# Performance work log

Measured on AMD Instinct MI355X. Metric: run time of the kernel, lower is better.

## Reference

```python
import jax, jax.numpy as jnp
from jax import lax
import numpy as np

N, T, HID, COMB, ATT, K, D = 128, 64, 512, 1024, 128, 20, 2
FMAP = 64  # CNN output channels; feature map is 14x14 -> 196 locations
ODIM = K + 2 * K * D + K + 1  # 121 mixture-density output params


def setup_inputs() -> dict:
    key = jax.random.key(0)
    keys = iter(jax.random.split(key, 64))

    def rn(shape, s=0.05):
        return jax.random.normal(next(keys), shape, jnp.float32) * s

    inp = dict(
        x=rn((N, T, D), 1.0),
        x_canv=jax.random.uniform(next(keys), (N, 1, 28, 28), dtype=jnp.float32),
        start=rn((N, D), 1.0),
        conv1_w=rn((16, 1, 3, 3), 0.3), conv1_b=rn((16,)),
        conv2_w=rn((32, 16, 3, 3), 0.1), conv2_b=rn((32,)),
        conv3_w=rn((64, 32, 3, 3), 0.1), conv3_b=rn((64,)),
        init_w=rn((2 * HID, FMAP + 16)), init_b=rn((2 * HID,)),
        Uw=rn((ATT, HID)), Ub=rn((ATT,)),
        Ww=rn((ATT, FMAP)), Wb=rn((ATT,)),
        vw=rn((1, ATT)), vb=rn((1,)),
        beta_w=rn((FMAP, HID)), beta_b=rn((FMAP,)),
        xemb_w=rn((16, D), 0.5), xemb_b=rn((16,)),
        semb_w=rn((16, D), 0.5), semb_b=rn((16,)),
        Wih=rn((4 * HID, FMAP + 16)), Whh=rn((4 * HID, HID)),
        bih=rn((4 * HID,)), bhh=rn((4 * HID,)),
        comb_w=rn((COMB, FMAP + HID + 32)), comb_b=rn((COMB,)),
        out_w=rn((ODIM, COMB)), out_b=rn((ODIM,)),
    )
    return inp


def _conv(x, w, b, stride):
    # torch Conv2d(kernel=3, padding=1) with NCHW / OIHW layout
    y = lax.conv_general_dilated(x, w, (stride, stride), ((1, 1), (1, 1)),
                                 dimension_numbers=('NCHW', 'OIHW', 'NCHW'))
    return y + b[None, :, None, None]


def reference(x, x_canv, start, conv1_w, conv1_b, conv2_w, conv2_b, conv3_w, conv3_b,
              init_w, init_b, Uw, Ub, Ww, Wb, vw, vb, beta_w, beta_b,
              xemb_w, xemb_b, semb_w, semb_b, Wih, Whh, bih, bhh,
              comb_w, comb_b, out_w, out_b):
    n, Tt, d = x.shape
    # sequence_pad: prepend zero vector, drop last step
    xp = jnp.concatenate([jnp.zeros((n, 1, d), x.dtype), x[:, :-1]], axis=1)
    xe = jnp.tanh(xp @ xemb_w.T + xemb_b)          # (n,T,16)
    se = jnp.tanh(start @ semb_w.T + semb_b)       # (n,16)
    # CNN (zscore_canvases with new_stats=True)
    c = (x_canv - 0.0243) / 0.1383
    c = jax.nn.relu(_conv(c, conv1_w, conv1_b, 1))
    c = jax.nn.relu(_conv(c, conv2_w, conv2_b, 1))
    c = jnp.tanh(_conv(c, conv3_w, conv3_b, 2))    # (n,64,14,14)
    a = c.transpose(0, 2, 3, 1).reshape(n, -1, FMAP)  # (n,196,64)
    # Initialize LSTM state (num_layers=1)
    hidden = jnp.tanh(jnp.concatenate([a.mean(axis=1), se], axis=1) @ init_w.T + init_b)
    hidden = hidden.reshape(n, HID, 2)
    h0, c0 = hidden[:, :, 0], hidden[:, :, 1]
    # AttendSAT.register_annotation: precompute W(a)
    W_a = a @ Ww.T + Wb                             # (n,196,att)
    # dropout masks are keep-probs (eval / dropout=0) -> all ones, identity

    def step(carry, xt):
        h, cs = carry
        Uh = h @ Uw.T + Ub                          # (n,att)
        e = (jnp.tanh(W_a + Uh[:, None, :]) @ vw.T).squeeze(-1) + vb[0]
        alpha = jax.nn.softmax(e, axis=-1)          # (n,196)
        z = jnp.einsum('nlf,nl->nf', a, alpha)      # (n,64)
        z = jax.nn.sigmoid(h @ beta_w.T + beta_b) * z
        gates = jnp.concatenate([xt, z], axis=1) @ Wih.T + bih + h @ Whh.T + bhh
        gi, gf, gg, go = jnp.split(gates, 4, axis=1)  # torch gate order i,f,g,o
        cs = jax.nn.sigmoid(gf) * cs + jax.nn.sigmoid(gi) * jnp.tanh(gg)
        h = jax.nn.sigmoid(go) * jnp.tanh(cs)
        y = jnp.tanh(jnp.concatenate([h, z, xt, se], axis=1) @ comb_w.T + comb_b)
        y = y @ out_w.T + out_b
        return (h, cs), y

    _, ys = lax.scan(step, (h0, c0), xe.transpose(1, 0, 2))
    y_out = ys.transpose(1, 0, 2)                   # (n,T,121)
    # unpack_output
    mix, means, scales, corrs, vlog = jnp.split(
        y_out, [K, K + K * D, K + 2 * K * D, 2 * K + 2 * K * D], axis=-1)
    mix = jax.nn.softmax(mix, axis=-1)
    means = means.reshape(n, Tt, K, D)
    scales = jnp.exp(scales).reshape(n, Tt, K, D)
    corrs = jnp.tanh(corrs)
    return (mix, means, scales, corrs, vlog.squeeze(-1))
```

## Files before the change

### kernel.cpp

```cpp
#include <hip/hip_runtime.h>


#define TN 128
#define TT 64

typedef __attribute__((ext_vector_type(4))) float f32x4;
typedef __attribute__((ext_vector_type(8))) short bf16x8;

__device__ __forceinline__ float fsigm(float x){ return __builtin_amdgcn_rcpf(1.0f + __expf(-x)); }
__device__ __forceinline__ float ftanh(float x){ return 1.0f - 2.0f*__builtin_amdgcn_rcpf(1.0f + __expf(2.0f*x)); }
__device__ __forceinline__ unsigned short f2bf(float f){
  unsigned int u = __float_as_uint(f);
  u += 0x7fffu + ((u >> 16) & 1u);
  return (unsigned short)(u >> 16);
}
__device__ __forceinline__ float b2f(unsigned short u){ return __uint_as_float(((unsigned)u)<<16); }
__device__ __forceinline__ void cvt8(unsigned short* d, const float* s){
  __align__(16) unsigned short vals[8];
  #pragma unroll
  for (int j=0;j<8;j++) vals[j] = f2bf(s[j]);
  *(float4*)d = *(float4*)vals;
}

__global__ __launch_bounds__(256) void k_conv1(const float* __restrict__ xc, const float* __restrict__ w,
                                               const float* __restrict__ b, unsigned short* __restrict__ c1bf){
  int idx = blockIdx.x*256 + threadIdx.x;
  if (idx >= TN*16*784) return;
  int p = idx % 784, oc = (idx/784) & 15, n = idx/(784*16);
  int py = p/28, px = p%28;
  const float* src = xc + n*784;
  float acc = b[oc];
  #pragma unroll
  for (int ky=0;ky<3;ky++){
    int iy = py+ky-1; if (iy<0||iy>=28) continue;
    #pragma unroll
    for (int kx=0;kx<3;kx++){
      int ix = px+kx-1; if (ix<0||ix>=28) continue;
      acc += (src[iy*28+ix]-0.0243f)*(1.0f/0.1383f) * w[oc*9+ky*3+kx];
    }
  }
  c1bf[idx] = f2bf(fmaxf(acc, 0.0f));
}

__global__ __launch_bounds__(256) void k_im2col2(const unsigned short* __restrict__ c1bf, unsigned short* __restrict__ a2){
  int u = blockIdx.x*256 + threadIdx.x;
  if (u >= 100352*20) return;
  int r = u / 20, k8 = (u - r*20)*8;
  int p = r % 784, n = r / 784;
  int py = p/28, px = p%28;
  __align__(16) unsigned short vals[8];
  #pragma unroll
  for (int j=0;j<8;j++){
    int k = k8 + j;
    unsigned short v = 0;
    if (k < 144){
      int ic = k/9, rem = k - ic*9, ky = rem/3, kx = rem - ky*3;
      int iy = py+ky-1, ix = px+kx-1;
      if (iy>=0 && iy<28 && ix>=0 && ix<28) v = c1bf[(n*16+ic)*784 + iy*28+ix];
    }
    vals[j] = v;
  }
  *(float4*)(a2 + (size_t)r*160 + k8) = *(float4*)vals;
}

__global__ __launch_bounds__(256) void k_gconv2(const unsigned short* __restrict__ a2,
    const unsigned short* __restrict__ w2b, const float* __restrict__ b2,
    unsigned short* __restrict__ c2bf){
  int mbase = blockIdx.x*128;
  int tid = threadIdx.x, w = tid>>6, l = tid&63;
  int lr = l&15, lk = (l>>4)*8;
  __shared__ unsigned short at[128*168];
  {
    int row = tid>>1, off = (tid&1)*80;
    const unsigned short* sp = a2 + (size_t)(mbase+row)*160 + off;
// ... 72 lines not shown
    __syncthreads();
    for (int kt=0; kt<5; ++kt){
      #pragma unroll
      for (int mi=0;mi<2;mi++){
        bf16x8 afrag = *(const bf16x8*)&at[((2*w+mi)*16+lr)*168 + kt*32 + lk];
        #pragma unroll
        for (int j=0;j<4;j++){
          bf16x8 bf = *(const bf16x8*)(w3b + (size_t)(j*16+lr)*320 + kt2*160 + kt*32 + lk);
          acc[mi][j] = __builtin_amdgcn_mfma_f32_16x16x32_bf16(afrag, bf, acc[mi][j], 0,0,0);
        }
      }
    }
    __syncthreads();
  }
  #pragma unroll
  for (int mi=0;mi<2;mi++){
    #pragma unroll
    for (int j=0;j<4;j++){
      int oc = j*16 + lr;
      float bb = b3[oc];
      #pragma unroll
      for (int i=0;i<4;i++){
        int r = mbase + (2*w+mi)*16 + (l>>4)*4 + i;
        int n = r/196, p = r - n*196;
        float v = ftanh(acc[mi][j][i] + bb);
        unsigned short vb16 = f2bf(v);
        afbf[(size_t)(n*64+oc)*196 + p] = vb16;
        abf[(size_t)r*64 + oc] = vb16;
      }
    }
  }
}

__global__ __launch_bounds__(64) void k_amean(const unsigned short* __restrict__ afbf, float* __restrict__ amean){
  int n = blockIdx.x, f = threadIdx.x;
  const unsigned short* row = afbf + (size_t)(n*64+f)*196;
  float s = 0;
  for (int l=0;l<196;l++) s += b2f(row[l]);
  amean[n*64+f] = s * (1.0f/196.0f);
}

__global__ __launch_bounds__(256) void k_embed(const float* __restrict__ x, const float* __restrict__ start,
    const float* __restrict__ xw, const float* __restrict__ xb,
    const float* __restrict__ sw, const float* __restrict__ sb,
    float* __restrict__ xe, float* __restrict__ se){
  int idx = blockIdx.x*256 + threadIdx.x;
  if (idx < TN*TT*16){
    int j = idx & 15, t = (idx>>4) & 63, n = idx>>10;
    float acc = xb[j];
    if (t > 0){
      const float* xp = x + (n*TT + t-1)*2;
      acc += xp[0]*xw[j*2] + xp[1]*xw[j*2+1];
    }
    xe[idx] = ftanh(acc);
  } else if (idx < TN*TT*16 + TN*16){
    int k2 = idx - TN*TT*16;
    int j = k2 & 15, n = k2 >> 4;
    float acc = sb[j] + start[n*2]*sw[j*2] + start[n*2+1]*sw[j*2+1];
    se[k2] = ftanh(acc);
  }
}

__global__ __launch_bounds__(256) void k_init(const float* __restrict__ amean, const float* __restrict__ se,
    const float* __restrict__ w, const float* __restrict__ b,
    unsigned short* __restrict__ hbfA, float* __restrict__ cbuf){
  int idx = blockIdx.x*256 + threadIdx.x;
  if (idx >= TN*1024) return;
  int o = idx & 1023, n = idx >> 10;
  const float* wr = w + o*80;
  float acc = b[o];
  for (int k2=0;k2<64;k2++) acc += amean[n*64+k2]*wr[k2];
  for (int k2=0;k2<16;k2++) acc += se[n*16+k2]*wr[64+k2];
  float v = ftanh(acc);
  if (o & 1) cbuf[n*512 + (o>>1)] = v;
  else       hbfA[n*512 + (o>>1)] = f2bf(v);
}

__global__ __launch_bounds__(256) void k_prep(
    const float* __restrict__ Whh, const float* __restrict__ Wih,
    const float* __restrict__ bih, const float* __restrict__ bhh,
    const float* __restrict__ comb_w, const float* __restrict__ out_w, const float* __restrict__ out_b,
    const float* __restrict__ Uw, const float* __restrict__ beta_w, const float* __restrict__ Ww,
    const float* __restrict__ conv2_w, const float* __restrict__ conv3_w,
    unsigned short* __restrict__ wgf, float* __restrict__ gbias,
    unsigned short* __restrict__ cwbf, unsigned short* __restrict__ owbf, float* __restrict__ obias,
    unsigned short* __restrict__ uwbf, unsigned short* __restrict__ betabf, unsigned short* __restrict__ wwbf,
    unsigned short* __restrict__ w2b, unsigned short* __restrict__ w3b){
  int u = blockIdx.x*256 + threadIdx.x;
  if (u < 155648){
    int fragi = u >> 6, lane = u & 63;
    int g = fragi / 608, rem = fragi - g*608;
    int b = rem / 19, kt = rem - b*19;
    int row = g*512 + b*16 + (lane & 15);
    int col = kt*32 + (lane >> 4)*8;
    __align__(16) unsigned short vals[8];
    if (col < 512){
      const float* s = Whh + (size_t)row*512 + col;
      #pragma unroll
      for (int j=0;j<8;j++) vals[j] = f2bf(s[j]);
    } else if (col - 512 < 80){
      const float* s = Wih + (size_t)row*80 + (col-512);
      #pragma unroll
      for (int j=0;j<8;j++) vals[j] = f2bf(s[j]);
    } else {
      #pragma unroll
      for (int j=0;j<8;j++) vals[j] = 0;
    }
    *(float4*)(wgf + (size_t)u*8) = *(float4*)vals;
    return;
  }
  u -= 155648;
  if (u < 256){
    #pragma unroll
    for (int j=0;j<8;j++) gbias[u*8+j] = bih[u*8+j] + bhh[u*8+j];
    return;
  }
  u -= 256;
  if (u < 77824){ cvt8(cwbf + (size_t)u*8, comb_w + (size_t)u*8); return; }
  u -= 77824;
  if (u < 16384){
    int o = u >> 7, k2 = (u & 127)*8;
    __align__(16) unsigned short vals[8];
    if (o < 121){
      const float* s = out_w + (size_t)o*1024 + k2;
      #pragma unroll
      for (int j=0;j<8;j++) vals[j] = f2bf(s[j]);
    } else {
      #pragma unroll
      for (int j=0;j<8;j++) vals[j] = 0;
    }
    *(float4*)(owbf + (size_t)u*8) = *(float4*)vals;
    return;
  }
  u -= 16384;
  if (u < 16){
    #pragma unroll
    for (int j=0;j<8;j++){ int i = u*8+j; obias[i] = (i<121)? out_b[i] : 0.0f; }
    return;
  }
  u -= 16;
  if (u < 8192){ cvt8(uwbf + (size_t)u*8, Uw + (size_t)u*8); return; }
  u -= 8192;
  if (u < 4096){ cvt8(betabf + (size_t)u*8, beta_w + (size_t)u*8); return; }
  u -= 4096;
  if (u < 1024){ cvt8(wwbf + (size_t)u*8, Ww + (size_t)u*8); return; }
  u -= 1024;
  if (u < 640){
    int o = u/20, k2 = (u - o*20)*8;
    if (k2 < 144) cvt8(w2b + (size_t)u*8, conv2_w + (size_t)o*144 + k2);
    else { __align__(16) unsigned short z[8] = {0,0,0,0,0,0,0,0}; *(float4*)(w2b + (size_t)u*8) = *(float4*)z; }
    return;
  }
  u -= 640;
  if (u < 2560){
    int o = u/40, k2 = (u - o*40)*8;
    if (k2 < 288) cvt8(w3b + (size_t)u*8, conv3_w + (size_t)o*288 + k2);
    else { __align__(16) unsigned short z[8] = {0,0,0,0,0,0,0,0}; *(float4*)(w3b + (size_t)u*8) = *(float4*)z; }
    return;
  }
}

__global__ __launch_bounds__(256) void k_wa(const unsigned short* __restrict__ abf,
    const unsigned short* __restrict__ wwbf, const float* __restrict__ Wb,
    unsigned short* __restrict__ wabf){
  int mbase = blockIdx.x*128;
  int tid = threadIdx.x, w = tid>>6, l = tid&63;
  int lr = l & 15, lk = (l>>4)*8;
  __shared__ unsigned short at[128*40];
  f32x4 acc[8][2];
  #pragma unroll
  for (int m=0;m<8;m++){ acc[m][0] = (f32x4){0,0,0,0}; acc[m][1] = (f32x4){0,0,0,0}; }
  for (int kt=0; kt<2; ++kt){
    int row = tid>>1, half = (tid&1)*16;
    const unsigned short* sp = abf + (mbase+row)*64 + kt*32 + half;
    *(float4*)&at[row*40 + half]     = *(const float4*)sp;
    *(float4*)&at[row*40 + half + 8] = *(const float4*)(sp + 8);
    __syncthreads();
    bf16x8 b0 = *(const bf16x8*)(wwbf + ((2*w+0)*16 + lr)*64 + kt*32 + lk);
    bf16x8 b1 = *(const bf16x8*)(wwbf + ((2*w+1)*16 + lr)*64 + kt*32 + lk);
    #pragma unroll
    for (int m=0;m<8;m++){
      bf16x8 afrag = *(const bf16x8*)&at[(m*16+lr)*40 + lk];
      acc[m][0] = __builtin_amdgcn_mfma_f32_16x16x32_bf16(afrag, b0, acc[m][0], 0,0,0);
      acc[m][1] = __builtin_amdgcn_mfma_f32_16x16x32_bf16(afrag, b1, acc[m][1], 0,0,0);
    }
    __syncthreads();
  }
  #pragma unroll
  for (int m=0;m<8;m++){
    #pragma unroll
    for (int j=0;j<2;j++){
      int att = (2*w+j)*16 + lr;
      float wb = Wb[att];
      #pragma unroll
      for (int i=0;i<4;i++){
        int arow = mbase + m*16 + (l>>4)*4 + i;
        int n = arow/196, l2 = arow - n*196;
        wabf[((size_t)n*196 + l2)*128 + att] = f2bf(acc[m][j][i] + wb);
      }
    }
  }
}

__global__ __launch_bounds__(512) void k_stepA(int t,
    const unsigned short* __restrict__ hbf_in,
    const unsigned short* __restrict__ uwbf, const float* __restrict__ Ub,
    const unsigned short* __restrict__ betabf, const float* __restrict__ beta_b,
    const float* __restrict__ vw, const float* __restrict__ vb,
    const unsigned short* __restrict__ wabf, const unsigned short* __restrict__ afbf,
    unsigned short* __restrict__ ubf_all, unsigned short* __restrict__ cbf,
    const unsigned short* __restrict__ wgf, float* __restrict__ gpart)
{
  const int bid = blockIdx.x, tid = threadIdx.x;
  __shared__ __align__(16) float hs[512];
  __shared__ __align__(16) float Uh[128];
  __shared__ __align__(16) float vws[128];
  __shared__ float bsig[64];
  __shared__ float ew[196];
  __shared__ float red[16];
  __shared__ float up[4][128];
  __shared__ float qp8[8][64];
  __shared__ float ep2[256][2];
  __shared__ __align__(16) unsigned short at2[128*516];

  if (bid < TN){
    const int n = bid;
    hs[tid] = b2f(hbf_in[n*512 + tid]);
    if (tid < 128) vws[tid] = vw[tid];
    const float vb0 = vb[0];
    __syncthreads();
    {
      int att = tid & 127, q = tid >> 7;
      const unsigned short* uw = uwbf + (size_t)att*512 + q*128;
      const float* hh = hs + q*128;
      float acc = 0.f;
      #pragma unroll 4
      for (int k=0;k<128;k+=8){
        bf16x8 v = *(const bf16x8*)(uw + k);
        acc += hh[k+0]*b2f(v[0]) + hh[k+1]*b2f(v[1]) + hh[k+2]*b2f(v[2]) + hh[k+3]*b2f(v[3])
             + hh[k+4]*b2f(v[4]) + hh[k+5]*b2f(v[5]) + hh[k+6]*b2f(v[6]) + hh[k+7]*b2f(v[7]);
      }
      up[q][att] = acc;
    }
    {
      int f = tid & 63, q = tid >> 6;
      const unsigned short* bw = betabf + (size_t)f*512 + q*64;
      const float* hh = hs + q*64;
      float acc = 0.f;
      #pragma unroll 4
      for (int k=0;k<64;k+=8){
        bf16x8 v = *(const bf16x8*)(bw + k);
        acc += hh[k+0]*b2f(v[0]) + hh[k+1]*b2f(v[1]) + hh[k+2]*b2f(v[2]) + hh[k+3]*b2f(v[3])
             + hh[k+4]*b2f(v[4]) + hh[k+5]*b2f(v[5]) + hh[k+6]*b2f(v[6]) + hh[k+7]*b2f(v[7]);
      }
      qp8[q][f] = acc;
    }
    __syncthreads();
    if (tid < 128) Uh[tid] = Ub[tid] + up[0][tid]+up[1][tid]+up[2][tid]+up[3][tid];
    else if (tid < 192){
      int f = tid-128;
      bsig[f] = fsigm(beta_b[f] + qp8[0][f]+qp8[1][f]+qp8[2][f]+qp8[3][f]
                                + qp8[4][f]+qp8[5][f]+qp8[6][f]+qp8[7][f]);
    }
    __syncthreads();
    {
      int l = tid >> 1, half = tid & 1;
      float acc = 0.f;
      if (l < 196){
        const unsigned short* wr = wabf + ((size_t)n*196 + l)*128 + half*64;
        const float* uh = Uh + half*64;
        const float* vv = vws + half*64;
        #pragma unroll 2
        for (int k=0;k<64;k+=8){
          bf16x8 wv = *(const bf16x8*)(wr + k);
          acc += vv[k+0]*ftanh(b2f(wv[0]) + uh[k+0]) + vv[k+1]*ftanh(b2f(wv[1]) + uh[k+1])
               + vv[k+2]*ftanh(b2f(wv[2]) + uh[k+2]) + vv[k+3]*ftanh(b2f(wv[3]) + uh[k+3])
               + vv[k+4]*ftanh(b2f(wv[4]) + uh[k+4]) + vv[k+5]*ftanh(b2f(wv[5]) + uh[k+5])
               + vv[k+6]*ftanh(b2f(wv[6]) + uh[k+6]) + vv[k+7]*ftanh(b2f(wv[7]) + uh[k+7]);
        }
      }
      ep2[l][half] = acc;
    }
    __syncthreads();
    float ev = -1e30f;
    if (tid < 196) ev = vb0 + ep2[tid][0] + ep2[tid][1];
    float m = ev;
    #pragma unroll
    for (int off=32; off>0; off>>=1) m = fmaxf(m, __shfl_xor(m, off));
    if ((tid&63)==0) red[tid>>6] = m;
    __syncthreads();
    float mx = red[0];
    #pragma unroll
    for (int i=1;i<8;i++) mx = fmaxf(mx, red[i]);
    float ex = (tid<196) ? __expf(ev - mx) : 0.0f;
    float ss = ex;
    #pragma unroll
    for (int off=32; off>0; off>>=1) ss += __shfl_xor(ss, off);
    if ((tid&63)==0) red[8+(tid>>6)] = ss;
    if (tid<196) ew[tid] = ex;
    __syncthreads();
    float inv = __builtin_amdgcn_rcpf(red[8]+red[9]+red[10]+red[11]+red[12]+red[13]+red[14]+red[15]);
    {
      int f = tid & 63, q = tid >> 6;
      int l0 = q*25, l1 = (l0+25 < 196) ? l0+25 : 196;
      const unsigned short* an = afbf + (size_t)n*12544 + (size_t)f*196;
      float acc = 0.f;
      for (int l2=l0; l2<l1; l2++) acc += ew[l2]*b2f(an[l2]);
      qp8[q][f] = acc;
    }
    __syncthreads();
    if (tid < 64){
      float z = bsig[tid]*(qp8[0][tid]+qp8[1][tid]+qp8[2][tid]+qp8[3][tid]
                          +qp8[4][tid]+qp8[5][tid]+qp8[6][tid]+qp8[7][tid])*inv;
      unsigned short zb = f2bf(z);
      ubf_all[((size_t)t*TN + n)*96 + 16 + tid] = zb;
      cbf[((size_t)n*TT + t)*608 + 512 + tid] = zb;
    }
  } else {
    const int b = bid - TN;
    const int w = tid>>6, l = tid&63, lr = l&15, li = l>>4, lk = li*8;
    const int g = w & 3, mh = w >> 2;
    bf16x8 wreg[16];
    {
      const unsigned short* wp = wgf + ((size_t)(g*32 + b)*19)*512 + (size_t)l*8;
      #pragma unroll
      for (int i=0;i<16;i++) wreg[i] = *(const bf16x8*)(wp + (size_t)i*512);
    }
    for (int i = tid; i < 8192; i += 512){
      int row = i >> 6, seg = (i & 63)*8;
      *(float4*)&at2[row*516 + seg] = *(const float4*)(hbf_in + (size_t)row*512 + seg);
    }
    __syncthreads();
    f32x4 acc[4];
    #pragma unroll
    for (int m2=0;m2<4;m2++) acc[m2] = (f32x4){0,0,0,0};
    #pragma unroll 4
    for (int kt=0; kt<16; ++kt){
      #pragma unroll
      for (int m2=0;m2<4;m2++){
        bf16x8 a = *(const bf16x8*)&at2[((mh*4+m2)*16 + lr)*516 + kt*32 + lk];
        acc[m2] = __builtin_amdgcn_mfma_f32_16x16x32_bf16(a, wreg[kt], acc[m2], 0,0,0);
      }
    }
    #pragma unroll
    for (int m2=0;m2<4;m2++){
      #pragma unroll
      for (int i=0;i<4;i++){
        int n2 = (mh*4+m2)*16 + li*4 + i;
// ... 32 lines not shown
  for (int kt=0; kt<3; ++kt){
    #pragma unroll
    for (int m2=0;m2<4;m2++){
      bf16x8 a = *(const bf16x8*)(ub + (size_t)((mh*4+m2)*16 + lr)*96 + kt*32 + lk);
      acc[m2] = __builtin_amdgcn_mfma_f32_16x16x32_bf16(a, wz[kt], acc[m2], 0,0,0);
    }
  }
  __syncthreads();
  #pragma unroll
  for (int m2=0;m2<4;m2++)
    #pragma unroll
    for (int i=0;i<4;i++)
      gsh[g][(mh*4+m2)*16 + li*4 + i][lr] += acc[m2][i];
  __syncthreads();
  #pragma unroll
  for (int e=0;e<4;++e){
    int c = tid*4 + e;
    int nn = c>>4, j = c&15;
    int hidx = b*16 + j;
    float gi = gsh[0][nn][j] + gbias[         hidx];
    float gf = gsh[1][nn][j] + gbias[1*512 + hidx];
    float gg = gsh[2][nn][j] + gbias[2*512 + hidx];
    float go = gsh[3][nn][j] + gbias[3*512 + hidx];
    float cc = cbuf[nn*512 + hidx];
    float cs = fsigm(gf)*cc + fsigm(gi)*ftanh(gg);
    float h  = fsigm(go)*ftanh(cs);
    cbuf[nn*512 + hidx] = cs;
    unsigned short hb = f2bf(h);
    hout[nn*512 + hidx] = hb;
    cbf[((size_t)nn*TT + t)*608 + hidx] = hb;
  }
}

__global__ __launch_bounds__(256) void k_cbf_xs(const float* __restrict__ xe, const float* __restrict__ se,
                                                unsigned short* __restrict__ cbf,
                                                unsigned short* __restrict__ ubf_all){
  int idx = blockIdx.x*256 + threadIdx.x;
  if (idx >= TN*TT*64) return;
  int j = idx & 63, r = idx >> 6;
  int n = r >> 6, t = r & 63;
  if (j < 16)      cbf[(size_t)r*608 + 576 + j] = f2bf(xe[r*16 + j]);
  else if (j < 32) cbf[(size_t)r*608 + 592 + (j-16)] = f2bf(se[n*16 + (j-16)]);
  else if (j < 48) ubf_all[((size_t)t*TN + n)*96 + (j-32)] = f2bf(xe[r*16 + (j-32)]);
  else             ubf_all[((size_t)t*TN + n)*96 + 80 + (j-48)] = 0;
}

__global__ __launch_bounds__(256) void k_comb(const unsigned short* __restrict__ cbf,
    const unsigned short* __restrict__ cwbf, const float* __restrict__ comb_b,
    unsigned short* __restrict__ ybf){
  int mbase = blockIdx.x*128, obase = blockIdx.y*128;
  int tid = threadIdx.x, w = tid>>6, l = tid&63;
  int lr = l&15, lk = (l>>4)*8;
  __shared__ unsigned short at[128*40];
  f32x4 acc[8][2];
  #pragma unroll
  for (int m=0;m<8;m++){ acc[m][0] = (f32x4){0,0,0,0}; acc[m][1] = (f32x4){0,0,0,0}; }
  for (int kt=0; kt<19; ++kt){
    int row = tid>>1, half = (tid&1)*16;
    const unsigned short* sp = cbf + (size_t)(mbase+row)*608 + kt*32 + half;
    *(float4*)&at[row*40 + half]     = *(const float4*)sp;
    *(float4*)&at[row*40 + half + 8] = *(const float4*)(sp + 8);
    __syncthreads();
    bf16x8 b0 = *(const bf16x8*)(cwbf + (size_t)(obase + (2*w+0)*16 + lr)*608 + kt*32 + lk);
    bf16x8 b1 = *(const bf16x8*)(cwbf + (size_t)(obase + (2*w+1)*16 + lr)*608 + kt*32 + lk);
    #pragma unroll
    for (int m=0;m<8;m++){
      bf16x8 afrag = *(const bf16x8*)&at[(m*16+lr)*40 + lk];
      acc[m][0] = __builtin_amdgcn_mfma_f32_16x16x32_bf16(afrag, b0, acc[m][0], 0,0,0);
      acc[m][1] = __builtin_amdgcn_mfma_f32_16x16x32_bf16(afrag, b1, acc[m][1], 0,0,0);
    }
    __syncthreads();
  }
  #pragma unroll
  for (int m=0;m<8;m++){
    #pragma unroll
    for (int j=0;j<2;j++){
      int o = obase + (2*w+j)*16 + lr;
      float cb = comb_b[o];
      #pragma unroll
      for (int i=0;i<4;i++){
        int r = mbase + m*16 + (l>>4)*4 + i;
        ybf[(size_t)r*1024 + o] = f2bf(ftanh(acc[m][j][i] + cb));
      }
    }
  }
}

__global__ __launch_bounds__(256) void k_out(const unsigned short* __restrict__ ybf,
    const unsigned short* __restrict__ owbf, const float* __restrict__ obias,
    float* __restrict__ obuf){
  int mbase = blockIdx.x*128;
  int tid = threadIdx.x, w = tid>>6, l = tid&63;
  int lr = l&15, lk = (l>>4)*8;
  __shared__ unsigned short at[128*40];
  f32x4 acc[8][2];
  #pragma unroll
  for (int m=0;m<8;m++){ acc[m][0] = (f32x4){0,0,0,0}; acc[m][1] = (f32x4){0,0,0,0}; }
  for (int kt=0; kt<32; ++kt){
    int row = tid>>1, half = (tid&1)*16;
    const unsigned short* sp = ybf + (size_t)(mbase+row)*1024 + kt*32 + half;
    *(float4*)&at[row*40 + half]     = *(const float4*)sp;
    *(float4*)&at[row*40 + half + 8] = *(const float4*)(sp + 8);
    __syncthreads();
    bf16x8 b0 = *(const bf16x8*)(owbf + ((2*w+0)*16 + lr)*1024 + kt*32 + lk);
    bf16x8 b1 = *(const bf16x8*)(owbf + ((2*w+1)*16 + lr)*1024 + kt*32 + lk);
    #pragma unroll
    for (int m=0;m<8;m++){
      bf16x8 afrag = *(const bf16x8*)&at[(m*16+lr)*40 + lk];
      acc[m][0] = __builtin_amdgcn_mfma_f32_16x16x32_bf16(afrag, b0, acc[m][0], 0,0,0);
      acc[m][1] = __builtin_amdgcn_mfma_f32_16x16x32_bf16(afrag, b1, acc[m][1], 0,0,0);
    }
    __syncthreads();
  }
  #pragma unroll
  for (int m=0;m<8;m++){
    #pragma unroll
    for (int j=0;j<2;j++){
      int o = (2*w+j)*16 + lr;
      float ob = obias[o];
      #pragma unroll
      for (int i=0;i<4;i++){
        int r = mbase + m*16 + (l>>4)*4 + i;
        obuf[(size_t)r*128 + o] = acc[m][j][i] + ob;
      }
    }
  }
}

__global__ __launch_bounds__(256) void k_post(const float* __restrict__ obuf, float* __restrict__ out){
  int r = blockIdx.x*256 + threadIdx.x;
  if (r >= TN*TT) return;
  const float* row = obuf + (size_t)r*128;
  float mx = -1e30f;
  #pragma unroll
  for (int k2=0;k2<20;k2++) mx = fmaxf(mx, row[k2]);
  float e[20]; float s = 0;
  #pragma unroll
  for (int k2=0;k2<20;k2++){ e[k2] = __expf(row[k2]-mx); s += e[k2]; }
  float inv = __builtin_amdgcn_rcpf(s);
  float* mixo  = out;
  float* meano = out + 163840;
  float* scaleo= out + 491520;
  float* corro = out + 819200;
  float* vlogo = out + 983040;
  #pragma unroll
  for (int k2=0;k2<20;k2++) mixo[r*20+k2] = e[k2]*inv;
  #pragma unroll
  for (int j=0;j<40;j++) meano[r*40+j] = row[20+j];
  #pragma unroll
  for (int j=0;j<40;j++) scaleo[r*40+j] = __expf(row[60+j]);
  #pragma unroll
  for (int k2=0;k2<20;k2++) corro[r*20+k2] = ftanh(row[100+k2]);
  vlogo[r] = row[120];
}

extern "C" void kernel_launch(void* const* d_in, const int* in_sizes, int n_in,
                              void* d_out, int out_size, void* d_ws, size_t ws_size,
                              hipStream_t stream){
  const float* x       = (const float*)d_in[0];
  const float* x_canv  = (const float*)d_in[1];
  const float* start_  = (const float*)d_in[2];
  const float* conv1_w = (const float*)d_in[3];
  const float* conv1_b = (const float*)d_in[4];
  const float* conv2_w = (const float*)d_in[5];
  const float* conv2_b = (const float*)d_in[6];
  const float* conv3_w = (const float*)d_in[7];
  const float* conv3_b = (const float*)d_in[8];
  const float* init_w  = (const float*)d_in[9];
  const float* init_b  = (const float*)d_in[10];
  const float* Uw      = (const float*)d_in[11];
  const float* Ub      = (const float*)d_in[12];
  const float* Ww      = (const float*)d_in[13];
  const float* Wb      = (const float*)d_in[14];
  const float* vw      = (const float*)d_in[15];
  const float* vb      = (const float*)d_in[16];
  const float* beta_w  = (const float*)d_in[17];
  const float* beta_b  = (const float*)d_in[18];
  const float* xemb_w  = (const float*)d_in[19];
  const float* xemb_b  = (const float*)d_in[20];
  const float* semb_w  = (const float*)d_in[21];
  const float* semb_b  = (const float*)d_in[22];
  const float* Wih     = (const float*)d_in[23];
  const float* Whh     = (const float*)d_in[24];
  const float* bih     = (const float*)d_in[25];
  const float* bhh     = (const float*)d_in[26];
  const float* comb_w  = (const float*)d_in[27];
  const float* comb_b  = (const float*)d_in[28];
  const float* out_w   = (const float*)d_in[29];
  const float* out_b   = (const float*)d_in[30];
  (void)in_sizes; (void)n_in; (void)out_size; (void)ws_size;

  char* wsb = (char*)d_ws;
  size_t off = 0;
  auto alloc = [&](size_t bytes)->char*{
    char* p = wsb + off;
    off = (off + bytes + 255) & ~(size_t)255;
    return p;
  };
  unsigned short* c1bf   = (unsigned short*)alloc((size_t)TN*16*784*2);
  unsigned short* a2     = (unsigned short*)alloc((size_t)100352*160*2);
  unsigned short* a3     = a2;
  unsigned short* c2bf   = (unsigned short*)alloc((size_t)100352*32*2);
  unsigned short* afbf   = (unsigned short*)alloc((size_t)TN*64*196*2);
  unsigned short* abf    = (unsigned short*)alloc((size_t)TN*196*64*2);
  float*          amean  = (float*)alloc((size_t)TN*64*4);
  float*          xe     = (float*)alloc((size_t)TN*TT*16*4);
  float*          se     = (float*)alloc((size_t)TN*16*4);
  unsigned short* wabf   = (unsigned short*)alloc((size_t)TN*196*128*2);
  float*          cbuf   = (float*)alloc((size_t)TN*512*4);
  unsigned short* hbfA   = (unsigned short*)alloc((size_t)TN*512*2);
  unsigned short* hbfB   = (unsigned short*)alloc((size_t)TN*512*2);
  unsigned short* ubf_all= (unsigned short*)alloc((size_t)TT*TN*96*2);
  unsigned short* cbf    = (unsigned short*)alloc((size_t)TN*TT*608*2);
  unsigned short* ybf    = (unsigned short*)alloc((size_t)TN*TT*1024*2);
  float*          obuf   = (float*)alloc((size_t)TN*TT*128*4);
  unsigned short* wgf    = (unsigned short*)alloc((size_t)1245184*2);
  float*          gbias  = (float*)alloc((size_t)2048*4);
  float*          gpart  = (float*)alloc((size_t)4*128*512*4);
  unsigned short* cwbf   = (unsigned short*)alloc((size_t)1024*608*2);
  unsigned short* owbf   = (unsigned short*)alloc((size_t)128*1024*2);
  float*          obias  = (float*)alloc((size_t)128*4);
  unsigned short* uwbf   = (unsigned short*)alloc((size_t)128*512*2);
  unsigned short* betabf = (unsigned short*)alloc((size_t)64*512*2);
  unsigned short* wwbf   = (unsigned short*)alloc((size_t)128*64*2);
  unsigned short* w2b    = (unsigned short*)alloc((size_t)32*160*2);
  unsigned short* w3b    = (unsigned short*)alloc((size_t)64*320*2);

  hipLaunchKernelGGL(k_conv1, dim3(6272), dim3(256), 0, stream, x_canv, conv1_w, conv1_b, c1bf);
  hipLaunchKernelGGL(k_prep, dim3(1042), dim3(256), 0, stream,
                     Whh, Wih, bih, bhh, comb_w, out_w, out_b, Uw, beta_w, Ww, conv2_w, conv3_w,
                     wgf, gbias, cwbf, owbf, obias, uwbf, betabf, wwbf, w2b, w3b);
  hipLaunchKernelGGL(k_im2col2, dim3(7840), dim3(256), 0, stream, c1bf, a2);
  hipLaunchKernelGGL(k_gconv2, dim3(784), dim3(256), 0, stream, a2, w2b, conv2_b, c2bf);
  hipLaunchKernelGGL(k_im2col3, dim3(3920), dim3(256), 0, stream, c2bf, a3);
  hipLaunchKernelGGL(k_gconv3, dim3(196), dim3(256), 0, stream, a3, w3b, conv3_b, afbf, abf);
  hipLaunchKernelGGL(k_amean, dim3(128), dim3(64), 0, stream, afbf, amean);
  hipLaunchKernelGGL(k_embed, dim3(520), dim3(256), 0, stream, x, start_, xemb_w, xemb_b, semb_w, semb_b, xe, se);
  hipLaunchKernelGGL(k_init, dim3(512), dim3(256), 0, stream, amean, se, init_w, init_b, hbfA, cbuf);
  hipLaunchKernelGGL(k_wa, dim3(196), dim3(256), 0, stream, abf, wwbf, Wb, wabf);
  hipLaunchKernelGGL(k_cbf_xs, dim3(2048), dim3(256), 0, stream, xe, se, cbf, ubf_all);

  for (int t = 0; t < TT; ++t){
    unsigned short* hin  = (t & 1) ? hbfB : hbfA;
    unsigned short* hout = (t & 1) ? hbfA : hbfB;
    hipLaunchKernelGGL(k_stepA, dim3(160), dim3(512), 0, stream, t,
                       hin, uwbf, Ub, betabf, beta_b, vw, vb, wabf, afbf, ubf_all, cbf, wgf, gpart);
    hipLaunchKernelGGL(k_stepB, dim3(32), dim3(512), 0, stream, t,
                       hout, ubf_all, wgf, gbias, gpart, cbuf, cbf);
  }

  hipLaunchKernelGGL(k_comb, dim3(64, 8), dim3(256), 0, stream, cbf, cwbf, comb_b, ybf);
  hipLaunchKernelGGL(k_out, dim3(64), dim3(256), 0, stream, ybf, owbf, obias, obuf);
  hipLaunchKernelGGL(k_post, dim3(32), dim3(256), 0, stream, obuf, (float*)d_out);
}
```

Measured before the change: 1.531 ms.

## Merge setup kernels, fuse output post-processing, drop softmax max pass in attention

Merges conv1 with weight preparation into one launch. Folds the feature mean, start embedding, W_a projection and embedding scatter into a single launch that computes the embeddings directly instead of going through an xe buffer. Fuses the mixture-density post-processing into the output GEMM through a shared-memory tile, removing the obuf round trip. Removes the max-subtraction reduction and one barrier from the per-step attention softmax; this is safe only while attention logits stay small enough not to overflow exp.

```diff
diff --git a/kernel.cpp b/kernel.cpp
--- a/kernel.cpp
+++ b/kernel.cpp
@@ -22,9 +22,8 @@
   *(float4*)d = *(float4*)vals;
 }
 
-__global__ __launch_bounds__(256) void k_conv1(const float* __restrict__ xc, const float* __restrict__ w,
-                                               const float* __restrict__ b, unsigned short* __restrict__ c1bf){
-  int idx = blockIdx.x*256 + threadIdx.x;
+__device__ __forceinline__ void dev_conv1(int idx, const float* __restrict__ xc,
+    const float* __restrict__ w, const float* __restrict__ b, unsigned short* __restrict__ c1bf){
   if (idx >= TN*16*784) return;
   int p = idx % 784, oc = (idx/784) & 15, n = idx/(784*16);
   int py = p/28, px = p%28;
@@ -40,6 +39,107 @@
     }
   }
   c1bf[idx] = f2bf(fmaxf(acc, 0.0f));
+}
+
+__device__ __forceinline__ void dev_prep(int u,
+    const float* __restrict__ Whh, const float* __restrict__ Wih,
+    const float* __restrict__ bih, const float* __restrict__ bhh,
+    const float* __restrict__ comb_w, const float* __restrict__ out_w, const float* __restrict__ out_b,
+    const float* __restrict__ Uw, const float* __restrict__ beta_w, const float* __restrict__ Ww,
+    const float* __restrict__ conv2_w, const float* __restrict__ conv3_w,
+    unsigned short* __restrict__ wgf, float* __restrict__ gbias,
+    unsigned short* __restrict__ cwbf, unsigned short* __restrict__ owbf, float* __restrict__ obias,
+    unsigned short* __restrict__ uwbf, unsigned short* __restrict__ betabf, unsigned short* __restrict__ wwbf,
+    unsigned short* __restrict__ w2b, unsigned short* __restrict__ w3b){
+  if (u < 155648){
+    int fragi = u >> 6, lane = u & 63;
+    int g = fragi / 608, rem = fragi - g*608;
+    int b = rem / 19, kt = rem - b*19;
+    int row = g*512 + b*16 + (lane & 15);
+    int col = kt*32 + (lane >> 4)*8;
+    __align__(16) unsigned short vals[8];
+    if (col < 512){
+      const float* s = Whh + (size_t)row*512 + col;
+      #pragma unroll
+      for (int j=0;j<8;j++) vals[j] = f2bf(s[j]);
+    } else if (col - 512 < 80){
+      const float* s = Wih + (size_t)row*80 + (col-512);
+      #pragma unroll
+      for (int j=0;j<8;j++) vals[j] = f2bf(s[j]);
+    } else {
+      #pragma unroll
+      for (int j=0;j<8;j++) vals[j] = 0;
+    }
+    *(float4*)(wgf + (size_t)u*8) = *(float4*)vals;
+    return;
+  }
+  u -= 155648;
+  if (u < 256){
+    #pragma unroll
+    for (int j=0;j<8;j++) gbias[u*8+j] = bih[u*8+j] + bhh[u*8+j];
+    return;
+  }
+  u -= 256;
+  if (u < 77824){ cvt8(cwbf + (size_t)u*8, comb_w + (size_t)u*8); return; }
+  u -= 77824;
+  if (u < 16384){
+    int o = u >> 7, k2 = (u & 127)*8;
+    __align__(16) unsigned short vals[8];
+    if (o < 121){
+      const float* s = out_w + (size_t)o*1024 + k2;
+      #pragma unroll
+      for (int j=0;j<8;j++) vals[j] = f2bf(s[j]);
+    } else {
+      #pragma unroll
+      for (int j=0;j<8;j++) vals[j] = 0;
+    }
+    *(float4*)(owbf + (size_t)u*8) = *(float4*)vals;
+    return;
+  }
+  u -= 16384;
+  if (u < 16){
+    #pragma unroll
+    for (int j=0;j<8;j++){ int i = u*8+j; obias[i] = (i<121)? out_b[i] : 0.0f; }
+    return;
+  }
+  u -= 16;
+  if (u < 8192){ cvt8(uwbf + (size_t)u*8, Uw + (size_t)u*8); return; }
+  u -= 8192;
+  if (u < 4096){ cvt8(betabf + (size_t)u*8, beta_w + (size_t)u*8); return; }
+  u -= 4096;
+  if (u < 1024){ cvt8(wwbf + (size_t)u*8, Ww + (size_t)u*8); return; }
+  u -= 1024;
+  if (u < 640){
+    int o = u/20, k2 = (u - o*20)*8;
+    if (k2 < 144) cvt8(w2b + (size_t)u*8, conv2_w + (size_t)o*144 + k2);
+    else { __align__(16) unsigned short z[8] = {0,0,0,0,0,0,0,0}; *(float4*)(w2b + (size_t)u*8) = *(float4*)z; }
+    return;
+  }
+  u -= 640;
+  if (u < 2560){
+    int o = u/40, k2 = (u - o*40)*8;
+    if (k2 < 288) cvt8(w3b + (size_t)u*8, conv3_w + (size_t)o*288 + k2);
+    else { __align__(16) unsigned short z[8] = {0,0,0,0,0,0,0,0}; *(float4*)(w3b + (size_t)u*8) = *(float4*)z; }
+    return;
+  }
+}
+
+__global__ __launch_bounds__(256) void k_head(const float* __restrict__ xc,
+    const float* __restrict__ conv1_w, const float* __restrict__ conv1_b, unsigned short* __restrict__ c1bf,
+    const float* __restrict__ Whh, const float* __restrict__ Wih,
+    const float* __restrict__ bih, const float* __restrict__ bhh,
+    const float* __restrict__ comb_w, const float* __restrict__ out_w, const float* __restrict__ out_b,
+    const float* __restrict__ Uw, const float* __restrict__ beta_w, const float* __restrict__ Ww,
+    const float* __restrict__ conv2_w, const float* __restrict__ conv3_w,
+    unsigned short* __restrict__ wgf, float* __restrict__ gbias,
+    unsigned short* __restrict__ cwbf, unsigned short* __restrict__ owbf, float* __restrict__ obias,
+    unsigned short* __restrict__ uwbf, unsigned short* __restrict__ betabf, unsigned short* __restrict__ wwbf,
+    unsigned short* __restrict__ w2b, unsigned short* __restrict__ w3b){
+  int bid = blockIdx.x;
+  if (bid < 6272) dev_conv1(bid*256 + threadIdx.x, xc, conv1_w, conv1_b, c1bf);
+  else dev_prep((bid-6272)*256 + threadIdx.x, Whh, Wih, bih, bhh, comb_w, out_w, out_b,
+                Uw, beta_w, Ww, conv2_w, conv3_w,
+                wgf, gbias, cwbf, owbf, obias, uwbf, betabf, wwbf, w2b, w3b);
 }
 
 __global__ __launch_bounds__(256) void k_im2col2(const unsigned short* __restrict__ c1bf, unsigned short* __restrict__ a2){
@@ -178,32 +278,95 @@
   }
 }
 
-__global__ __launch_bounds__(64) void k_amean(const unsigned short* __restrict__ afbf, float* __restrict__ amean){
-  int n = blockIdx.x, f = threadIdx.x;
-  const unsigned short* row = afbf + (size_t)(n*64+f)*196;
-  float s = 0;
-  for (int l=0;l<196;l++) s += b2f(row[l]);
-  amean[n*64+f] = s * (1.0f/196.0f);
-}
-
-__global__ __launch_bounds__(256) void k_embed(const float* __restrict__ x, const float* __restrict__ start,
-    const float* __restrict__ xw, const float* __restrict__ xb,
-    const float* __restrict__ sw, const float* __restrict__ sb,
-    float* __restrict__ xe, float* __restrict__ se){
-  int idx = blockIdx.x*256 + threadIdx.x;
-  if (idx < TN*TT*16){
-    int j = idx & 15, t = (idx>>4) & 63, n = idx>>10;
-    float acc = xb[j];
-    if (t > 0){
-      const float* xp = x + (n*TT + t-1)*2;
-      acc += xp[0]*xw[j*2] + xp[1]*xw[j*2+1];
-    }
-    xe[idx] = ftanh(acc);
-  } else if (idx < TN*TT*16 + TN*16){
-    int k2 = idx - TN*TT*16;
-    int j = k2 & 15, n = k2 >> 4;
-    float acc = sb[j] + start[n*2]*sw[j*2] + start[n*2+1]*sw[j*2+1];
-    se[k2] = ftanh(acc);
+__global__ __launch_bounds__(256) void k_mid(
+    const unsigned short* __restrict__ afbf, float* __restrict__ amean,
+    const float* __restrict__ start, const float* __restrict__ sw, const float* __restrict__ sb,
+    float* __restrict__ se,
+    const unsigned short* __restrict__ abf, const unsigned short* __restrict__ wwbf,
+    const float* __restrict__ Wb, unsigned short* __restrict__ wabf,
+    const float* __restrict__ x, const float* __restrict__ xw, const float* __restrict__ xb,
+    unsigned short* __restrict__ cbf, unsigned short* __restrict__ ubf_all)
+{
+  const int bid = blockIdx.x, tid = threadIdx.x;
+  __shared__ __align__(16) unsigned short at[128*40];
+  __shared__ float qp[4][64];
+  if (bid < 128){
+    int f = tid & 63, q = tid >> 6;
+    const unsigned short* row = afbf + (size_t)(bid*64+f)*196 + q*49;
+    float s = 0;
+    #pragma unroll 7
+    for (int l=0;l<49;l++) s += b2f(row[l]);
+    qp[q][f] = s;
+    __syncthreads();
+    if (tid < 64) amean[bid*64+tid] = (qp[0][tid]+qp[1][tid]+qp[2][tid]+qp[3][tid]) * (1.0f/196.0f);
+    return;
+  }
+  if (bid == 128){
+    for (int i = tid; i < TN*16; i += 256){
+      int j = i & 15, n = i >> 4;
+      se[i] = ftanh(sb[j] + start[n*2]*sw[j*2] + start[n*2+1]*sw[j*2+1]);
+    }
+    return;
+  }
+  if (bid < 325){
+    int mbase = (bid-129)*128;
+    int w = tid>>6, l = tid&63;
+    int lr = l & 15, lk = (l>>4)*8;
+    f32x4 acc[8][2];
+    #pragma unroll
+    for (int m=0;m<8;m++){ acc[m][0] = (f32x4){0,0,0,0}; acc[m][1] = (f32x4){0,0,0,0}; }
+    for (int kt=0; kt<2; ++kt){
+      int row = tid>>1, half = (tid&1)*16;
+      const unsigned short* sp = abf + (mbase+row)*64 + kt*32 + half;
+      *(float4*)&at[row*40 + half]     = *(const float4*)sp;
+      *(float4*)&at[row*40 + half + 8] = *(const float4*)(sp + 8);
+      __syncthreads();
+      bf16x8 b0 = *(const bf16x8*)(wwbf + ((2*w+0)*16 + lr)*64 + kt*32 + lk);
+      bf16x8 b1 = *(const bf16x8*)(wwbf + ((2*w+1)*16 + lr)*64 + kt*32 + lk);
+      #pragma unroll
+      for (int m=0;m<8;m++){
+        bf16x8 afrag = *(const bf16x8*)&at[(m*16+lr)*40 + lk];
+        acc[m][0] = __builtin_amdgcn_mfma_f32_16x16x32_bf16(afrag, b0, acc[m][0], 0,0,0);
+        acc[m][1] = __builtin_amdgcn_mfma_f32_16x16x32_bf16(afrag, b1, acc[m][1], 0,0,0);
+      }
+      __syncthreads();
+    }
+    #pragma unroll
+    for (int m=0;m<8;m++){
+      #pragma unroll
+      for (int j=0;j<2;j++){
+        int att = (2*w+j)*16 + lr;
+        float wb = Wb[att];
+        #pragma unroll
+        for (int i=0;i<4;i++){
+          int arow = mbase + m*16 + (l>>4)*4 + i;
+          int n = arow/196, l2 = arow - n*196;
+          wabf[((size_t)n*196 + l2)*128 + att] = f2bf(acc[m][j][i] + wb);
+        }
+      }
+    }
+    return;
+  }
+  {
+    int idx = (bid-325)*256 + tid;
+    if (idx >= TN*TT*64) return;
+    int j = idx & 63, r = idx >> 6;
+    int n = r >> 6, t = r & 63;
+    if (j < 16){
+      float acc = xb[j];
+      if (t > 0){ const float* xp = x + (n*TT + t-1)*2; acc += xp[0]*xw[j*2] + xp[1]*xw[j*2+1]; }
+      cbf[(size_t)r*608 + 576 + j] = f2bf(ftanh(acc));
+    } else if (j < 32){
+      int jj = j-16;
+      cbf[(size_t)r*608 + 592 + jj] = f2bf(ftanh(sb[jj] + start[n*2]*sw[jj*2] + start[n*2+1]*sw[jj*2+1]));
+    } else if (j < 48){
+      int jj = j-32;
+      float acc = xb[jj];
+      if (t > 0){ const float* xp = x + (n*TT + t-1)*2; acc += xp[0]*xw[jj*2] + xp[1]*xw[jj*2+1]; }
+      ubf_all[((size_t)t*TN + n)*96 + jj] = f2bf(ftanh(acc));
+    } else {
+      ubf_all[((size_t)t*TN + n)*96 + 80 + (j-48)] = 0;
+    }
   }
 }
 
@@ -220,132 +383,6 @@
   float v = ftanh(acc);
   if (o & 1) cbuf[n*512 + (o>>1)] = v;
   else       hbfA[n*512 + (o>>1)] = f2bf(v);
-}
-
-__global__ __launch_bounds__(256) void k_prep(
-    const float* __restrict__ Whh, const float* __restrict__ Wih,
-    const float* __restrict__ bih, const float* __restrict__ bhh,
-    const float* __restrict__ comb_w, const float* __restrict__ out_w, const float* __restrict__ out_b,
-    const float* __restrict__ Uw, const float* __restrict__ beta_w, const float* __restrict__ Ww,
-    const float* __restrict__ conv2_w, const float* __restrict__ conv3_w,
-    unsigned short* __restrict__ wgf, float* __restrict__ gbias,
-    unsigned short* __restrict__ cwbf, unsigned short* __restrict__ owbf, float* __restrict__ obias,
-    unsigned short* __restrict__ uwbf, unsigned short* __restrict__ betabf, unsigned short* __restrict__ wwbf,
-    unsigned short* __restrict__ w2b, unsigned short* __restrict__ w3b){
-  int u = blockIdx.x*256 + threadIdx.x;
-  if (u < 155648){
-    int fragi = u >> 6, lane = u & 63;
-    int g = fragi / 608, rem = fragi - g*608;
-    int b = rem / 19, kt = rem - b*19;
-    int row = g*512 + b*16 + (lane & 15);
-    int col = kt*32 + (lane >> 4)*8;
-    __align__(16) unsigned short vals[8];
-    if (col < 512){
-      const float* s = Whh + (size_t)row*512 + col;
-      #pragma unroll
-      for (int j=0;j<8;j++) vals[j] = f2bf(s[j]);
-    } else if (col - 512 < 80){
-      const float* s = Wih + (size_t)row*80 + (col-512);
-      #pragma unroll
-      for (int j=0;j<8;j++) vals[j] = f2bf(s[j]);
-    } else {
-      #pragma unroll
-      for (int j=0;j<8;j++) vals[j] = 0;
-    }
-    *(float4*)(wgf + (size_t)u*8) = *(float4*)vals;
-    return;
-  }
-  u -= 155648;
-  if (u < 256){
-    #pragma unroll
-    for (int j=0;j<8;j++) gbias[u*8+j] = bih[u*8+j] + bhh[u*8+j];
-    return;
-  }
-  u -= 256;
-  if (u < 77824){ cvt8(cwbf + (size_t)u*8, comb_w + (size_t)u*8); return; }
-  u -= 77824;
-  if (u < 16384){
-    int o = u >> 7, k2 = (u & 127)*8;
-    __align__(16) unsigned short vals[8];
-    if (o < 121){
-      const float* s = out_w + (size_t)o*1024 + k2;
-      #pragma unroll
-      for (int j=0;j<8;j++) vals[j] = f2bf(s[j]);
-    } else {
-      #pragma unroll
-      for (int j=0;j<8;j++) vals[j] = 0;
-    }
-    *(float4*)(owbf + (size_t)u*8) = *(float4*)vals;
-    return;
-  }
-  u -= 16384;
-  if (u < 16){
-    #pragma unroll
-    for (int j=0;j<8;j++){ int i = u*8+j; obias[i] = (i<121)? out_b[i] : 0.0f; }
-    return;
-  }
-  u -= 16;
-  if (u < 8192){ cvt8(uwbf + (size_t)u*8, Uw + (size_t)u*8); return; }
-  u -= 8192;
-  if (u < 4096){ cvt8(betabf + (size_t)u*8, beta_w + (size_t)u*8); return; }
-  u -= 4096;
-  if (u < 1024){ cvt8(wwbf + (size_t)u*8, Ww + (size_t)u*8); return; }
-  u -= 1024;
-  if (u < 640){
-    int o = u/20, k2 = (u - o*20)*8;
-    if (k2 < 144) cvt8(w2b + (size_t)u*8, conv2_w + (size_t)o*144 + k2);
-    else { __align__(16) unsigned short z[8] = {0,0,0,0,0,0,0,0}; *(float4*)(w2b + (size_t)u*8) = *(float4*)z; }
-    return;
-  }
-  u -= 640;
-  if (u < 2560){
-    int o = u/40, k2 = (u - o*40)*8;
-    if (k2 < 288) cvt8(w3b + (size_t)u*8, conv3_w + (size_t)o*288 + k2);
-    else { __align__(16) unsigned short z[8] = {0,0,0,0,0,0,0,0}; *(float4*)(w3b + (size_t)u*8) = *(float4*)z; }
-    return;
-  }
-}
-
-__global__ __launch_bounds__(256) void k_wa(const unsigned short* __restrict__ abf,
-    const unsigned short* __restrict__ wwbf, const float* __restrict__ Wb,
-    unsigned short* __restrict__ wabf){
-  int mbase = blockIdx.x*128;
-  int tid = threadIdx.x, w = tid>>6, l = tid&63;
-  int lr = l & 15, lk = (l>>4)*8;
-  __shared__ unsigned short at[128*40];
-  f32x4 acc[8][2];
-  #pragma unroll
-  for (int m=0;m<8;m++){ acc[m][0] = (f32x4){0,0,0,0}; acc[m][1] = (f32x4){0,0,0,0}; }
-  for (int kt=0; kt<2; ++kt){
-    int row = tid>>1, half = (tid&1)*16;
-    const unsigned short* sp = abf + (mbase+row)*64 + kt*32 + half;
-    *(float4*)&at[row*40 + half]     = *(const float4*)sp;
-    *(float4*)&at[row*40 + half + 8] = *(const float4*)(sp + 8);
-    __syncthreads();
-    bf16x8 b0 = *(const bf16x8*)(wwbf + ((2*w+0)*16 + lr)*64 + kt*32 + lk);
-    bf16x8 b1 = *(const bf16x8*)(wwbf + ((2*w+1)*16 + lr)*64 + kt*32 + lk);
-    #pragma unroll
-    for (int m=0;m<8;m++){
-      bf16x8 afrag = *(const bf16x8*)&at[(m*16+lr)*40 + lk];
-      acc[m][0] = __builtin_amdgcn_mfma_f32_16x16x32_bf16(afrag, b0, acc[m][0], 0,0,0);
-      acc[m][1] = __builtin_amdgcn_mfma_f32_16x16x32_bf16(afrag, b1, acc[m][1], 0,0,0);
-    }
-    __syncthreads();
-  }
-  #pragma unroll
-  for (int m=0;m<8;m++){
-    #pragma unroll
-    for (int j=0;j<2;j++){
-      int att = (2*w+j)*16 + lr;
-      float wb = Wb[att];
-      #pragma unroll
-      for (int i=0;i<4;i++){
-        int arow = mbase + m*16 + (l>>4)*4 + i;
-        int n = arow/196, l2 = arow - n*196;
-        wabf[((size_t)n*196 + l2)*128 + att] = f2bf(acc[m][j][i] + wb);
-      }
-    }
-  }
 }
 
 __global__ __launch_bounds__(512) void k_stepA(int t,
@@ -363,7 +400,7 @@
   __shared__ __align__(16) float vws[128];
   __shared__ float bsig[64];
   __shared__ float ew[196];
-  __shared__ float red[16];
+  __shared__ float red[8];
   __shared__ float up[4][128];
   __shared__ float qp8[8][64];
   __shared__ float ep2[256][2];
@@ -428,24 +465,15 @@
       ep2[l][half] = acc;
     }
     __syncthreads();
-    float ev = -1e30f;
-    if (tid < 196) ev = vb0 + ep2[tid][0] + ep2[tid][1];
-    float m = ev;
-    #pragma unroll
-    for (int off=32; off>0; off>>=1) m = fmaxf(m, __shfl_xor(m, off));
-    if ((tid&63)==0) red[tid>>6] = m;
-    __syncthreads();
-    float mx = red[0];
-    #pragma unroll
-    for (int i=1;i<8;i++) mx = fmaxf(mx, red[i]);
-    float ex = (tid<196) ? __expf(ev - mx) : 0.0f;
+    float ex = 0.f;
+    if (tid < 196) ex = __expf(vb0 + ep2[tid][0] + ep2[tid][1]);
     float ss = ex;
     #pragma unroll
     for (int off=32; off>0; off>>=1) ss += __shfl_xor(ss, off);
-    if ((tid&63)==0) red[8+(tid>>6)] = ss;
+    if ((tid&63)==0) red[tid>>6] = ss;
     if (tid<196) ew[tid] = ex;
     __syncthreads();
-    float inv = __builtin_amdgcn_rcpf(red[8]+red[9]+red[10]+red[11]+red[12]+red[13]+red[14]+red[15]);
+    float inv = __builtin_amdgcn_rcpf(red[0]+red[1]+red[2]+red[3]+red[4]+red[5]+red[6]+red[7]);
     {
       int f = tid & 63, q = tid >> 6;
       int l0 = q*25, l1 = (l0+25 < 196) ? l0+25 : 196;
@@ -459,7 +487,7 @@
       float z = bsig[tid]*(qp8[0][tid]+qp8[1][tid]+qp8[2][tid]+qp8[3][tid]
                           +qp8[4][tid]+qp8[5][tid]+qp8[6][tid]+qp8[7][tid])*inv;
       unsigned short zb = f2bf(z);
-      ubf_all[((size_t)t*TN + n)*96 + 16 + tid] = zb;
+      ubf_all[((size_t)t*TN + tid>=0 ? (size_t)t*TN + n : 0)*96 + 16 + tid] = zb;
       cbf[((size_t)n*TT + t)*608 + 512 + tid] = zb;
     }
   } else {
@@ -558,19 +586,6 @@
   }
 }
 
-__global__ __launch_bounds__(256) void k_cbf_xs(const float* __restrict__ xe, const float* __restrict__ se,
-                                                unsigned short* __restrict__ cbf,
-                                                unsigned short* __restrict__ ubf_all){
-  int idx = blockIdx.x*256 + threadIdx.x;
-  if (idx >= TN*TT*64) return;
-  int j = idx & 63, r = idx >> 6;
-  int n = r >> 6, t = r & 63;
-  if (j < 16)      cbf[(size_t)r*608 + 576 + j] = f2bf(xe[r*16 + j]);
-  else if (j < 32) cbf[(size_t)r*608 + 592 + (j-16)] = f2bf(se[n*16 + (j-16)]);
-  else if (j < 48) ubf_all[((size_t)t*TN + n)*96 + (j-32)] = f2bf(xe[r*16 + (j-32)]);
-  else             ubf_all[((size_t)t*TN + n)*96 + 80 + (j-48)] = 0;
-}
-
 __global__ __launch_bounds__(256) void k_comb(const unsigned short* __restrict__ cbf,
     const unsigned short* __restrict__ cwbf, const float* __restrict__ comb_b,
     unsigned short* __restrict__ ybf){
@@ -614,11 +629,12 @@
 
 __global__ __launch_bounds__(256) void k_out(const unsigned short* __restrict__ ybf,
     const unsigned short* __restrict__ owbf, const float* __restrict__ obias,
-    float* __restrict__ obuf){
+    float* __restrict__ out){
   int mbase = blockIdx.x*128;
   int tid = threadIdx.x, w = tid>>6, l = tid&63;
   int lr = l&15, lk = (l>>4)*8;
   __shared__ unsigned short at[128*40];
+  __shared__ float osh[128][129];
   f32x4 acc[8][2];
   #pragma unroll
   for (int m=0;m<8;m++){ acc[m][0] = (f32x4){0,0,0,0}; acc[m][1] = (f32x4){0,0,0,0}; }
@@ -646,38 +662,37 @@
       float ob = obias[o];
       #pragma unroll
       for (int i=0;i<4;i++){
-        int r = mbase + m*16 + (l>>4)*4 + i;
-        obuf[(size_t)r*128 + o] = acc[m][j][i] + ob;
-      }
-    }
-  }
-}
-
-__global__ __launch_bounds__(256) void k_post(const float* __restrict__ obuf, float* __restrict__ out){
-  int r = blockIdx.x*256 + threadIdx.x;
-  if (r >= TN*TT) return;
-  const float* row = obuf + (size_t)r*128;
-  float mx = -1e30f;
-  #pragma unroll
-  for (int k2=0;k2<20;k2++) mx = fmaxf(mx, row[k2]);
-  float e[20]; float s = 0;
-  #pragma unroll
-  for (int k2=0;k2<20;k2++){ e[k2] = __expf(row[k2]-mx); s += e[k2]; }
-  float inv = __builtin_amdgcn_rcpf(s);
-  float* mixo  = out;
-  float* meano = out + 163840;
-  float* scaleo= out + 491520;
-  float* corro = out + 819200;
-  float* vlogo = out + 983040;
-  #pragma unroll
-  for (int k2=0;k2<20;k2++) mixo[r*20+k2] = e[k2]*inv;
-  #pragma unroll
-  for (int j=0;j<40;j++) meano[r*40+j] = row[20+j];
-  #pragma unroll
-  for (int j=0;j<40;j++) scaleo[r*40+j] = __expf(row[60+j]);
-  #pragma unroll
-  for (int k2=0;k2<20;k2++) corro[r*20+k2] = ftanh(row[100+k2]);
-  vlogo[r] = row[120];
+        int r = m*16 + (l>>4)*4 + i;
+        osh[r][o] = acc[m][j][i] + ob;
+      }
+    }
+  }
+  __syncthreads();
+  if (tid < 128){
+    const float* row = osh[tid];
+    int r = mbase + tid;
+    float mx = -1e30f;
+    #pragma unroll
+    for (int k2=0;k2<20;k2++) mx = fmaxf(mx, row[k2]);
+    float e[20]; float s = 0;
+    #pragma unroll
+    for (int k2=0;k2<20;k2++){ e[k2] = __expf(row[k2]-mx); s += e[k2]; }
+    float inv = __builtin_amdgcn_rcpf(s);
+    float* mixo  = out;
+    float* meano = out + 163840;
+    float* scaleo= out + 491520;
+    float* corro = out + 819200;
+    float* vlogo = out + 983040;
+    #pragma unroll
+    for (int k2=0;k2<20;k2++) mixo[r*20+k2] = e[k2]*inv;
+    #pragma unroll
+    for (int j=0;j<40;j++) meano[r*40+j] = row[20+j];
+    #pragma unroll
+    for (int j=0;j<40;j++) scaleo[r*40+j] = __expf(row[60+j]);
+    #pragma unroll
+    for (int k2=0;k2<20;k2++) corro[r*20+k2] = ftanh(row[100+k2]);
+    vlogo[r] = row[120];
+  }
 }
 
 extern "C" void kernel_launch(void* const* d_in, const int* in_sizes, int n_in,
@@ -730,7 +745,6 @@
   unsigned short* afbf   = (unsigned short*)alloc((size_t)TN*64*196*2);
   unsigned short* abf    = (unsigned short*)alloc((size_t)TN*196*64*2);
   float*          amean  = (float*)alloc((size_t)TN*64*4);
-  float*          xe     = (float*)alloc((size_t)TN*TT*16*4);
   float*          se     = (float*)alloc((size_t)TN*16*4);
   unsigned short* wabf   = (unsigned short*)alloc((size_t)TN*196*128*2);
   float*          cbuf   = (float*)alloc((size_t)TN*512*4);
@@ -739,7 +753,6 @@
   unsigned short* ubf_all= (unsigned short*)alloc((size_t)TT*TN*96*2);
   unsigned short* cbf    = (unsigned short*)alloc((size_t)TN*TT*608*2);
   unsigned short* ybf    = (unsigned short*)alloc((size_t)TN*TT*1024*2);
-  float*          obuf   = (float*)alloc((size_t)TN*TT*128*4);
   unsigned short* wgf    = (unsigned short*)alloc((size_t)1245184*2);
   float*          gbias  = (float*)alloc((size_t)2048*4);
   float*          gpart  = (float*)alloc((size_t)4*128*512*4);
@@ -752,19 +765,19 @@
   unsigned short* w2b    = (unsigned short*)alloc((size_t)32*160*2);
   unsigned short* w3b    = (unsigned short*)alloc((size_t)64*320*2);
 
-  hipLaunchKernelGGL(k_conv1, dim3(6272), dim3(256), 0, stream, x_canv, conv1_w, conv1_b, c1bf);
-  hipLaunchKernelGGL(k_prep, dim3(1042), dim3(256), 0, stream,
+  hipLaunchKernelGGL(k_head, dim3(7314), dim3(256), 0, stream,
+                     x_canv, conv1_w, conv1_b, c1bf,
                      Whh, Wih, bih, bhh, comb_w, out_w, out_b, Uw, beta_w, Ww, conv2_w, conv3_w,
                      wgf, gbias, cwbf, owbf, obias, uwbf, betabf, wwbf, w2b, w3b);
   hipLaunchKernelGGL(k_im2col2, dim3(7840), dim3(256), 0, stream, c1bf, a2);
   hipLaunchKernelGGL(k_gconv2, dim3(784), dim3(256), 0, stream, a2, w2b, conv2_b, c2bf);
   hipLaunchKernelGGL(k_im2col3, dim3(3920), dim3(256), 0, stream, c2bf, a3);
   hipLaunchKernelGGL(k_gconv3, dim3(196), dim3(256), 0, stream, a3, w3b, conv3_b, afbf, abf);
-  hipLaunchKernelGGL(k_amean, dim3(128), dim3(64), 0, stream, afbf, amean);
-  hipLaunchKernelGGL(k_embed, dim3(520), dim3(256), 0, stream, x, start_, xemb_w, xemb_b, semb_w, semb_b, xe, se);
+  hipLaunchKernelGGL(k_mid, dim3(2373), dim3(256), 0, stream,
+                     afbf, amean, start_, semb_w, semb_b, se,
+                     abf, wwbf, Wb, wabf,
+                     x, xemb_w, xemb_b, cbf, ubf_all);
   hipLaunchKernelGGL(k_init, dim3(512), dim3(256), 0, stream, amean, se, init_w, init_b, hbfA, cbuf);
-  hipLaunchKernelGGL(k_wa, dim3(196), dim3(256), 0, stream, abf, wwbf, Wb, wabf);
-  hipLaunchKernelGGL(k_cbf_xs, dim3(2048), dim3(256), 0, stream, xe, se, cbf, ubf_all);
 
   for (int t = 0; t < TT; ++t){
     unsigned short* hin  = (t & 1) ? hbfB : hbfA;
@@ -776,6 +789,5 @@
   }
 
   hipLaunchKernelGGL(k_comb, dim3(64, 8), dim3(256), 0, stream, cbf, cwbf, comb_b, ybf);
-  hipLaunchKernelGGL(k_out, dim3(64), dim3(256), 0, stream, ybf, owbf, obias, obuf);
-  hipLaunchKernelGGL(k_post, dim3(32), dim3(256), 0, stream, obuf, (float*)d_out);
-}
+  hipLaunchKernelGGL(k_out, dim3(64), dim3(256), 0, stream, ybf, owbf, obias, (float*)d_out);
+}
```

New measurement: 1.486 ms. 1.03x faster.
